# Kernel tuning notes

Measured on AMD Instinct MI355X. Metric: run time of the kernel, lower is better.

Reference implementation:

```python
import jax, jax.numpy as jnp
import numpy as np

B, T, C, H = 8, 1024, 1536, 12
D = C // H  # head_size = 128
EPS = 1e-5


def layer_norm(x, g, b):
    m = jnp.mean(x, axis=-1, keepdims=True)
    v = jnp.var(x, axis=-1, keepdims=True)
    return (x - m) / jnp.sqrt(v + EPS) * g + b


def batch_norm_T(x, g, b):
    # BatchNorm1d(block_size) on (B, T, C): channels are the T axis;
    # training-mode batch statistics over (B, C), biased variance.
    m = jnp.mean(x, axis=(0, 2), keepdims=True)
    v = jnp.var(x, axis=(0, 2), keepdims=True)
    return (x - m) / jnp.sqrt(v + EPS) * g[None, :, None] + b[None, :, None]


def setup_inputs() -> dict:
    key = jax.random.key(0)
    ks = jax.random.split(key, 12)
    s = 0.02
    inp = {
        "x": jax.random.normal(ks[0], (B, T, C), dtype=jnp.float32),
        # per-head q/k/v projections stacked: (H, C, D)
        "wq": jax.random.normal(ks[1], (H, C, D), dtype=jnp.float32) * s,
        "wk": jax.random.normal(ks[2], (H, C, D), dtype=jnp.float32) * s,
        "wv": jax.random.normal(ks[3], (H, C, D), dtype=jnp.float32) * s,
        "wo": jax.random.normal(ks[4], (C, C), dtype=jnp.float32) * s,
        "bo": jnp.zeros((C,), dtype=jnp.float32),
        "ln1_g": jnp.ones((C,), dtype=jnp.float32),
        "ln1_b": jnp.zeros((C,), dtype=jnp.float32),
        "ln2_g": jnp.ones((C,), dtype=jnp.float32),
        "ln2_b": jnp.zeros((C,), dtype=jnp.float32),
        "w1": jax.random.normal(ks[5], (C, 4 * C), dtype=jnp.float32) * s,
        "b1": jnp.zeros((4 * C,), dtype=jnp.float32),
        "w2": jax.random.normal(ks[6], (4 * C, C), dtype=jnp.float32) * s,
        "b2": jnp.zeros((C,), dtype=jnp.float32),
        "bn1_g": jnp.ones((T,), dtype=jnp.float32),
        "bn1_b": jnp.zeros((T,), dtype=jnp.float32),
        "bn2_g": jnp.ones((T,), dtype=jnp.float32),
        "bn2_b": jnp.zeros((T,), dtype=jnp.float32),
    }
    return inp


def reference(x, wq, wk, wv, wo, bo, ln1_g, ln1_b, ln2_g, ln2_b,
              w1, b1, w2, b2, bn1_g, bn1_b, bn2_g, bn2_b):
    # --- multi-head causal self-attention (pre-LN) ---
    h = layer_norm(x, ln1_g, ln1_b)                       # (B,T,C)
    q = jnp.einsum('btc,hcd->bhtd', h, wq)
    k = jnp.einsum('btc,hcd->bhtd', h, wk)
    v = jnp.einsum('btc,hcd->bhtd', h, wv)
    scores = jnp.einsum('bhtd,bhsd->bhts', q, k) * (D ** -0.5)
    causal = jnp.tril(jnp.ones((T, T), dtype=bool))
    scores = jnp.where(causal, scores, -jnp.inf)
    attn = jax.nn.softmax(scores, axis=-1)                # dropout = identity (eval)
    o = jnp.einsum('bhts,bhsd->bthd', attn, v).reshape(B, T, C)
    sa = o @ wo + bo
    x = x + sa
    x = batch_norm_T(x, bn1_g, bn1_b)
    # --- feed-forward ---
    h2 = layer_norm(x, ln2_g, ln2_b)
    ff = jax.nn.relu(h2 @ w1 + b1) @ w2 + b2
    x = batch_norm_T(x + ff, bn2_g, bn2_b)
    return x
```

## Files before the change

kernel.cpp:

```cpp
#include <hip/hip_runtime.h>
#include <hip/hip_bf16.h>

constexpr int BATCH = 8;
constexpr int SEQ   = 1024;
constexpr int CH    = 1536;
constexpr int NH    = 12;
constexpr int HD    = 128;
constexpr int FFDIM = 6144;
constexpr int NROWS = BATCH * SEQ;
constexpr int QKVLD = 3 * CH;
constexpr float EPS = 1e-5f;

typedef unsigned short ushort;
typedef __attribute__((ext_vector_type(8))) ushort us8;
typedef __attribute__((ext_vector_type(8))) __bf16 bf16x8;
typedef __attribute__((ext_vector_type(4))) float f32x4;

__device__ __forceinline__ float b2f(ushort u) {
  return __uint_as_float(((unsigned)u) << 16);
}
__device__ __forceinline__ ushort f2b(float f) {
  __hip_bfloat16 h = __float2bfloat16(f);
  return *reinterpret_cast<ushort*>(&h);
}

__device__ __forceinline__ void g2l16(const ushort* g, ushort* l) {
  __builtin_amdgcn_global_load_lds(
      (const __attribute__((address_space(1))) void*)g,
      (__attribute__((address_space(3))) void*)l, 16, 0, 0);
}

__device__ __forceinline__ float block_sum(float v, float* red) {
#pragma unroll
  for (int o = 32; o > 0; o >>= 1) v += __shfl_down(v, o, 64);
  const int w = threadIdx.x >> 6;
  if ((threadIdx.x & 63) == 0) red[w] = v;
  __syncthreads();
  const float r = red[0] + red[1] + red[2] + red[3];
  __syncthreads();
  return r;
}

__global__ __launch_bounds__(256) void ln_bf16(const float* __restrict__ x,
                                               const float* __restrict__ g,
                                               const float* __restrict__ b,
                                               ushort* __restrict__ out) {
  __shared__ float row[CH];
  __shared__ float red[4];
  const size_t base = (size_t)blockIdx.x * CH;
  float s = 0.f;
  for (int c = threadIdx.x; c < CH; c += 256) {
    const float v = x[base + c];
    row[c] = v;
    s += v;
  }
  const float mean = block_sum(s, red) * (1.0f / CH);
  float s2 = 0.f;
  for (int c = threadIdx.x; c < CH; c += 256) {
    const float d = row[c] - mean;
    s2 += d * d;
  }
  const float var = block_sum(s2, red) * (1.0f / CH);
  const float rstd = rsqrtf(var + EPS);
  for (int c = threadIdx.x; c < CH; c += 256)
    out[base + c] = f2b((row[c] - mean) * rstd * g[c] + b[c]);
}

__global__ __launch_bounds__(256) void transpose_cast(const float* __restrict__ src,
                                                      ushort* __restrict__ dst,
                                                      int R, int Cc, int ldd,
                                                      long srcZ, long dstZ) {
  __shared__ float tile[32][33];
  src += (size_t)blockIdx.z * srcZ;
  dst += (size_t)blockIdx.z * dstZ;
  const int c0 = blockIdx.x * 32, r0 = blockIdx.y * 32;
  const int tx = threadIdx.x & 31, ty = threadIdx.x >> 5;
#pragma unroll
  for (int i = ty; i < 32; i += 8)
    tile[i][tx] = src[(size_t)(r0 + i) * Cc + c0 + tx];
  __syncthreads();
#pragma unroll
  for (int i = ty; i < 32; i += 8)
    dst[(size_t)(c0 + i) * ldd + r0 + tx] = f2b(tile[tx][i]);
}

__global__ __launch_bounds__(256) void transpose_v(const ushort* __restrict__ src,
                                                   ushort* __restrict__ dst) {
  __shared__ ushort tile[32][33];
  const int bh = blockIdx.z;
  const int b = bh / NH, h = bh % NH;
  const ushort* s = src + (size_t)b * SEQ * QKVLD + (size_t)h * HD;
  ushort* d = dst + (size_t)bh * HD * SEQ;
  const int t0 = blockIdx.x * 32, d0 = blockIdx.y * 32;
  const int tx = threadIdx.x & 31, ty = threadIdx.x >> 5;
#pragma unroll
  for (int i = ty; i < 32; i += 8)
    tile[i][tx] = s[(size_t)(t0 + i) * QKVLD + d0 + tx];
  __syncthreads();
#pragma unroll
  for (int i = ty; i < 32; i += 8)
    d[(size_t)(d0 + i) * SEQ + t0 + tx] = tile[tx][i];
}

constexpr int BT = 128;
constexpr int BK = 32;

template <int RELU, int BIAS, int RES, int OUTBF>
__global__ __launch_bounds__(256) void gemm_bf16(
    const ushort* __restrict__ A, int lda,
    const ushort* __restrict__ Bt, int ldb,
    void* __restrict__ Cm, int ldc,
    const float* __restrict__ bias,
    const float* __restrict__ res, int ldr,
    int K) {
  __shared__ ushort As[BT * BK];
  __shared__ ushort Bs[BT * BK];
  const int tid = threadIdx.x;
  const int lane = tid & 63;
  const int wv = tid >> 6;
  const int m0 = blockIdx.y * BT;
  const int n0 = blockIdx.x * BT;
  const int srow = wv * 32 + (lane >> 2);
  const int schunk = (lane & 3) * 8;
  const ushort* gA0 = A + (size_t)(m0 + srow) * lda + schunk;
  const ushort* gA1 = gA0 + (size_t)16 * lda;
  const ushort* gB0 = Bt + (size_t)(n0 + srow) * ldb + schunk;
  const ushort* gB1 = gB0 + (size_t)16 * ldb;
  ushort* lA0 = As + (wv * 32) * BK;
  ushort* lA1 = lA0 + 16 * BK;
  ushort* lB0 = Bs + (wv * 32) * BK;
  ushort* lB1 = lB0 + 16 * BK;
  const int wm = (wv >> 1) * 64, wn = (wv & 1) * 64;
  const int fr = lane & 15;
  const int quad = lane >> 4;
  const int koff = quad * 8;

  f32x4 acc[4][4] = {{}};
  for (int k0 = 0; k0 < K; k0 += BK) {
    __syncthreads();
    g2l16(gA0 + k0, lA0);
    g2l16(gA1 + k0, lA1);
    g2l16(gB0 + k0, lB0);
    g2l16(gB1 + k0, lB1);
    __syncthreads();
    bf16x8 af[4], bf[4];
#pragma unroll
    for (int mi = 0; mi < 4; ++mi)
      af[mi] = *(const bf16x8*)&As[(wm + mi * 16 + fr) * BK + koff];
#pragma unroll
    for (int ni = 0; ni < 4; ++ni)
      bf[ni] = *(const bf16x8*)&Bs[(wn + ni * 16 + fr) * BK + koff];
#pragma unroll
    for (int mi = 0; mi < 4; ++mi)
#pragma unroll
      for (int ni = 0; ni < 4; ++ni)
        acc[mi][ni] = __builtin_amdgcn_mfma_f32_16x16x32_bf16(af[mi], bf[ni], acc[mi][ni], 0, 0, 0);
  }
#pragma unroll
  for (int ni = 0; ni < 4; ++ni) {
    const int col = n0 + wn + ni * 16 + fr;
    const float bs = BIAS ? bias[col] : 0.f;
#pragma unroll
    for (int mi = 0; mi < 4; ++mi) {
      const int rowb = m0 + wm + mi * 16 + quad * 4;
#pragma unroll
      for (int r = 0; r < 4; ++r) {
        float v = acc[mi][ni][r] + bs;
        if (RELU) v = fmaxf(v, 0.f);
        const size_t idx = (size_t)(rowb + r) * ldc + col;
        if (RES) v += res[(size_t)(rowb + r) * ldr + col];
        if (OUTBF) ((ushort*)Cm)[idx] = f2b(v);
        else       ((float*)Cm)[idx] = v;
      }
    }
  }
}

constexpr int FQT = 64;
constexpr int VLD = 72;

__global__ __launch_bounds__(256) void flash_attn_mfma(
    const ushort* __restrict__ q, const ushort* __restrict__ k,
    const ushort* __restrict__ vt, ushort* __restrict__ o,
    int ld, int ldo) {
  __shared__ ushort Ks[2][64 * 128];
  __shared__ ushort Vs[2][128 * 64];
  __shared__ ushort Ps[4][16][VLD];
  const int tid = threadIdx.x;
  const int lane = tid & 63;
  const int w = tid >> 6;
  const int fr = lane & 15;
  const int quad = lane >> 4;
  const int qt = blockIdx.x;
  const int b = blockIdx.y / NH;
  const int h = blockIdx.y % NH;
  const size_t base = (size_t)b * SEQ * ld + (size_t)h * HD;
  const ushort* vtb = vt + (size_t)(b * NH + h) * HD * SEQ;
  const int q0 = qt * FQT;
  const int qrow = q0 + w * 16;
  const float scale = 0.08838834764831845f;

  const ushort* gk[4];
  const ushort* gv[4];
#pragma unroll
  for (int t = 0; t < 4; ++t) {
    const int jr = w * 16 + t * 4 + (lane >> 4);
    const int kc = (lane & 15) ^ (jr & 7);
    gk[t] = k + base + (size_t)jr * ld + kc * 8;
    const int dr = w * 32 + t * 8 + (lane >> 3);
    const int vc = (lane & 7) ^ (dr & 7);
    gv[t] = vtb + (size_t)dr * SEQ + vc * 8;
  }

  bf16x8 aq[4];
  {
    const ushort* qp = q + base + (size_t)(qrow + fr) * ld + quad * 8;
#pragma unroll
    for (int ks = 0; ks < 4; ++ks) aq[ks] = *(const bf16x8*)(qp + ks * 32);
  }

  float m_i[4], l_i[4];
  f32x4 oacc[8];
#pragma unroll
  for (int i = 0; i < 4; ++i) { m_i[i] = -3.0e38f; l_i[i] = 0.f; }
#pragma unroll
  for (int n8 = 0; n8 < 8; ++n8) oacc[n8] = (f32x4){0.f, 0.f, 0.f, 0.f};

#pragma unroll
  for (int t = 0; t < 4; ++t) {
    g2l16(gk[t], &Ks[0][w * 2048 + t * 512]);
    g2l16(gv[t], &Vs[0][w * 2048 + t * 512]);
  }
  __syncthreads();

  int cur = 0;
  for (int jt = 0; jt <= qt; ++jt) {
    const int j0 = jt * FQT;
    if (jt < qt) {
      const size_t ko = (size_t)(jt + 1) * FQT * ld;
      const int vo = (jt + 1) * FQT;
      ushort* kd = (cur ? &Ks[0][0] : &Ks[1][0]) + w * 2048;
      ushort* vd = (cur ? &Vs[0][0] : &Vs[1][0]) + w * 2048;
#pragma unroll
      for (int t = 0; t < 4; ++t) {
        g2l16(gk[t] + ko, kd + t * 512);
        g2l16(gv[t] + vo, vd + t * 512);
      }
    }
    const ushort* Kc = cur ? &Ks[1][0] : &Ks[0][0];
    const ushort* Vc = cur ? &Vs[1][0] : &Vs[0][0];

    f32x4 sacc[4];
#pragma unroll
    for (int ni = 0; ni < 4; ++ni) sacc[ni] = (f32x4){0.f, 0.f, 0.f, 0.f};
#pragma unroll
    for (int ks = 0; ks < 4; ++ks) {
#pragma unroll
      for (int ni = 0; ni < 4; ++ni) {
        const int j = ni * 16 + fr;
        const int s = (ks * 4 + quad) ^ (fr & 7);
        const bf16x8 kf = *(const bf16x8*)&Kc[j * 128 + s * 8];
        sacc[ni] = __builtin_amdgcn_mfma_f32_16x16x32_bf16(aq[ks], kf, sacc[ni], 0, 0, 0);
      }
    }
    const bool diag = (jt == qt);
    float alpha[4];
#pragma unroll
    for (int i = 0; i < 4; ++i) {
      const int qg = qrow + quad * 4 + i;
      float pv[4];
      float vmax = -3.0e38f;
#pragma unroll
      for (int ni = 0; ni < 4; ++ni) {
        float sv = sacc[ni][i] * scale;
        if (diag && (j0 + ni * 16 + fr > qg)) sv = -3.0e38f;
        pv[ni] = sv;
        vmax = fmaxf(vmax, sv);
      }
#pragma unroll
      for (int mm = 8; mm >= 1; mm >>= 1) vmax = fmaxf(vmax, __shfl_xor(vmax, mm, 64));
      const float m_new = fmaxf(m_i[i], vmax);
      alpha[i] = __expf(m_i[i] - m_new);
      m_i[i] = m_new;
      float rsum = 0.f;
#pragma unroll
      for (int ni = 0; ni < 4; ++ni) {
        const float pe = __expf(pv[ni] - m_new);
        Ps[w][quad * 4 + i][ni * 16 + fr] = f2b(pe);
        rsum += pe;
      }
#pragma unroll
      for (int mm = 8; mm >= 1; mm >>= 1) rsum += __shfl_xor(rsum, mm, 64);
      l_i[i] = l_i[i] * alpha[i] + rsum;
#pragma unroll
      for (int n8 = 0; n8 < 8; ++n8) oacc[n8][i] *= alpha[i];
    }
#pragma unroll
    for (int js = 0; js < 2; ++js) {
      const bf16x8 pf = *(const bf16x8*)&Ps[w][fr][js * 32 + quad * 8];
#pragma unroll
      for (int n8 = 0; n8 < 8; ++n8) {
        const int d = n8 * 16 + fr;
        const int s = (js * 4 + quad) ^ (fr & 7);
        const bf16x8 vf = *(const bf16x8*)&Vc[d * 64 + s * 8];
        oacc[n8] = __builtin_amdgcn_mfma_f32_16x16x32_bf16(pf, vf, oacc[n8], 0, 0, 0);
      }
    }
    __syncthreads();
    cur ^= 1;
  }
#pragma unroll
  for (int i = 0; i < 4; ++i) {
    const float inv = 1.0f / l_i[i];
    ushort* op = o + ((size_t)b * SEQ + qrow + quad * 4 + i) * ldo + (size_t)h * HD;
#pragma unroll
    for (int n8 = 0; n8 < 8; ++n8) op[n8 * 16 + fr] = f2b(oacc[n8][i] * inv);
  }
}

__global__ __launch_bounds__(256) void bn_stats(const float* __restrict__ x,
                                                float* __restrict__ mean,
                                                float* __restrict__ rstd) {
  __shared__ float red[4];
  const int t = blockIdx.x;
  float s = 0.f;
  for (int bb = 0; bb < BATCH; ++bb) {
    const float* p = x + ((size_t)bb * SEQ + t) * CH;
    for (int c = threadIdx.x; c < CH; c += 256) s += p[c];
  }
  const float m = block_sum(s, red) * (1.0f / (BATCH * CH));
  float s2 = 0.f;
  for (int bb = 0; bb < BATCH; ++bb) {
    const float* p = x + ((size_t)bb * SEQ + t) * CH;
    for (int c = threadIdx.x; c < CH; c += 256) {
      const float d = p[c] - m;
      s2 += d * d;
    }
  }
  const float var = block_sum(s2, red) * (1.0f / (BATCH * CH));
  if (threadIdx.x == 0) {
    mean[t] = m;
    rstd[t] = rsqrtf(var + EPS);
  }
}

__global__ __launch_bounds__(256) void bn_apply(const float* __restrict__ x,
                                                float* __restrict__ out,
                                                const float* __restrict__ mean,
                                                const float* __restrict__ rstd,
                                                const float* __restrict__ g,
                                                const float* __restrict__ bb) {
  const size_t i = (size_t)blockIdx.x * 256 + threadIdx.x;
  const int t = (int)((i / CH) % SEQ);
  out[i] = (x[i] - mean[t]) * rstd[t] * g[t] + bb[t];
}

extern "C" void kernel_launch(void* const* d_in, const int* in_sizes, int n_in,
                              void* d_out, int out_size, void* d_ws, size_t ws_size,
                              hipStream_t stream) {
  const float* x    = (const float*)d_in[0];
  const float* wq   = (const float*)d_in[1];
  const float* wk   = (const float*)d_in[2];
  const float* wv   = (const float*)d_in[3];
  const float* wo   = (const float*)d_in[4];
  const float* bo   = (const float*)d_in[5];
  const float* ln1g = (const float*)d_in[6];
  const float* ln1b = (const float*)d_in[7];
  const float* ln2g = (const float*)d_in[8];
  const float* ln2b = (const float*)d_in[9];
  const float* w1   = (const float*)d_in[10];
  const float* b1   = (const float*)d_in[11];
  const float* w2   = (const float*)d_in[12];
  const float* b2   = (const float*)d_in[13];
  const float* bn1g = (const float*)d_in[14];
  const float* bn1b = (const float*)d_in[15];
  const float* bn2g = (const float*)d_in[16];
  const float* bn2b = (const float*)d_in[17];
  float* out = (float*)d_out;

  ushort* wsu = (ushort*)d_ws;
  const size_t NCs   = (size_t)NROWS * CH;
  ushort* R0    = wsu;
  ushort* QKV   = wsu + NCs;
  ushort* wqkvT = wsu + NCs + (size_t)NROWS * QKVLD;
  ushort* woT   = wqkvT + (size_t)QKVLD * CH;
  float*  meanp = (float*)(woT + (size_t)CH * CH);
  float*  rstdp = meanp + SEQ;
  ushort* w1T   = QKV;
  ushort* w2T   = QKV + (size_t)FFDIM * CH;
  ushort* FF1   = QKV + 2 * (size_t)FFDIM * CH;

  const dim3 blk(256);

  transpose_cast<<<dim3(HD / 32, CH / 32, NH), blk, 0, stream>>>(
      wq, wqkvT, CH, HD, CH, (long)CH * HD, (long)HD * CH);
  transpose_cast<<<dim3(HD / 32, CH / 32, NH), blk, 0, stream>>>(
      wk, wqkvT + (size_t)CH * CH, CH, HD, CH, (long)CH * HD, (long)HD * CH);
  transpose_cast<<<dim3(HD / 32, CH / 32, NH), blk, 0, stream>>>(
      wv, wqkvT + 2 * (size_t)CH * CH, CH, HD, CH, (long)CH * HD, (long)HD * CH);
  transpose_cast<<<dim3(CH / 32, CH / 32, 1), blk, 0, stream>>>(
      wo, woT, CH, CH, CH, 0, 0);

  ln_bf16<<<NROWS, blk, 0, stream>>>(x, ln1g, ln1b, R0);

  gemm_bf16<0, 0, 0, 1><<<dim3(QKVLD / BT, NROWS / BT), blk, 0, stream>>>(
      R0, CH, wqkvT, CH, QKV, QKVLD, nullptr, nullptr, 0, CH);

  transpose_v<<<dim3(SEQ / 32, HD / 32, BATCH * NH), blk, 0, stream>>>(
      QKV + 2 * CH, R0);

  flash_attn_mfma<<<dim3(SEQ / FQT, BATCH * NH), blk, 0, stream>>>(
      QKV, QKV + CH, R0, QKV, QKVLD, QKVLD);

  gemm_bf16<0, 1, 1, 0><<<dim3(CH / BT, NROWS / BT), blk, 0, stream>>>(
      QKV, QKVLD, woT, CH, out, CH, bo, x, CH, CH);

  transpose_cast<<<dim3(FFDIM / 32, CH / 32, 1), blk, 0, stream>>>(
      w1, w1T, CH, FFDIM, CH, 0, 0);
  transpose_cast<<<dim3(CH / 32, FFDIM / 32, 1), blk, 0, stream>>>(
      w2, w2T, FFDIM, CH, FFDIM, 0, 0);

  bn_stats<<<SEQ, blk, 0, stream>>>(out, meanp, rstdp);
  bn_apply<<<(NROWS * CH) / 256, blk, 0, stream>>>(out, out, meanp, rstdp, bn1g, bn1b);

  ln_bf16<<<NROWS, blk, 0, stream>>>(out, ln2g, ln2b, R0);

  constexpr int FFC = 4096;
  for (int c = 0; c < NROWS / FFC; ++c) {
    const size_t r0 = (size_t)c * FFC;
    gemm_bf16<1, 1, 0, 1><<<dim3(FFDIM / BT, FFC / BT), blk, 0, stream>>>(
        R0 + r0 * CH, CH, w1T, CH, FF1, FFDIM, b1, nullptr, 0, CH);
    gemm_bf16<0, 1, 1, 0><<<dim3(CH / BT, FFC / BT), blk, 0, stream>>>(
        FF1, FFDIM, w2T, FFDIM, out + r0 * CH, CH, b2, out + r0 * CH, CH, FFDIM);
  }

  bn_stats<<<SEQ, blk, 0, stream>>>(out, meanp, rstdp);
  bn_apply<<<(NROWS * CH) / 256, blk, 0, stream>>>(out, out, meanp, rstdp, bn2g, bn2b);
}
```

Baseline: 1.277 ms.

## Double-buffer GEMM LDS tiles, swizzle LDS layout, split-K FFN2 with atomics

The bf16 GEMM now prefetches the next K tile into a second LDS buffer while computing the current one, with one barrier per iteration instead of two. LDS chunk offsets are XOR-swizzled by row to reduce bank conflicts on fragment reads. The second FFN GEMM is split along K into two slices that atomically accumulate into the output, which already holds the residual; only the first slice adds bias. The split raises block count for the under-filled GEMM but adds atomic traffic and makes the summation order nondeterministic.

```diff
diff --git a/kernel.cpp b/kernel.cpp
--- a/kernel.cpp
+++ b/kernel.cpp
@@ -105,7 +105,7 @@
 constexpr int BT = 128;
 constexpr int BK = 32;
 
-template <int RELU, int BIAS, int RES, int OUTBF>
+template <int RELU, int BIAS, int RES, int OUTBF, int ATOMIC = 0>
 __global__ __launch_bounds__(256) void gemm_bf16(
     const ushort* __restrict__ A, int lda,
     const ushort* __restrict__ Bt, int ldb,
@@ -113,53 +113,65 @@
     const float* __restrict__ bias,
     const float* __restrict__ res, int ldr,
     int K) {
-  __shared__ ushort As[BT * BK];
-  __shared__ ushort Bs[BT * BK];
+  __shared__ ushort As[2][BT * BK];
+  __shared__ ushort Bs[2][BT * BK];
   const int tid = threadIdx.x;
   const int lane = tid & 63;
   const int wv = tid >> 6;
   const int m0 = blockIdx.y * BT;
   const int n0 = blockIdx.x * BT;
+  if (ATOMIC) {
+    const size_t kz = (size_t)blockIdx.z * K;
+    A += kz;
+    Bt += kz;
+  }
   const int srow = wv * 32 + (lane >> 2);
-  const int schunk = (lane & 3) * 8;
+  const int sx = (srow >> 1) & 3;
+  const int schunk = ((lane & 3) ^ sx) * 8;
   const ushort* gA0 = A + (size_t)(m0 + srow) * lda + schunk;
   const ushort* gA1 = gA0 + (size_t)16 * lda;
   const ushort* gB0 = Bt + (size_t)(n0 + srow) * ldb + schunk;
   const ushort* gB1 = gB0 + (size_t)16 * ldb;
-  ushort* lA0 = As + (wv * 32) * BK;
-  ushort* lA1 = lA0 + 16 * BK;
-  ushort* lB0 = Bs + (wv * 32) * BK;
-  ushort* lB1 = lB0 + 16 * BK;
+  const int lofs = (wv * 32) * BK;
   const int wm = (wv >> 1) * 64, wn = (wv & 1) * 64;
   const int fr = lane & 15;
   const int quad = lane >> 4;
-  const int koff = quad * 8;
+  const int koff = (quad ^ ((fr >> 1) & 3)) * 8;
 
   f32x4 acc[4][4] = {{}};
+  g2l16(gA0, &As[0][lofs]);
+  g2l16(gA1, &As[0][lofs + 16 * BK]);
+  g2l16(gB0, &Bs[0][lofs]);
+  g2l16(gB1, &Bs[0][lofs + 16 * BK]);
+  __syncthreads();
+  int buf = 0;
   for (int k0 = 0; k0 < K; k0 += BK) {
-    __syncthreads();
-    g2l16(gA0 + k0, lA0);
-    g2l16(gA1 + k0, lA1);
-    g2l16(gB0 + k0, lB0);
-    g2l16(gB1 + k0, lB1);
-    __syncthreads();
+    const int nk = k0 + BK;
+    if (nk < K) {
+      g2l16(gA0 + nk, &As[buf ^ 1][lofs]);
+      g2l16(gA1 + nk, &As[buf ^ 1][lofs + 16 * BK]);
+      g2l16(gB0 + nk, &Bs[buf ^ 1][lofs]);
+      g2l16(gB1 + nk, &Bs[buf ^ 1][lofs + 16 * BK]);
+    }
     bf16x8 af[4], bf[4];
 #pragma unroll
     for (int mi = 0; mi < 4; ++mi)
-      af[mi] = *(const bf16x8*)&As[(wm + mi * 16 + fr) * BK + koff];
+      af[mi] = *(const bf16x8*)&As[buf][(wm + mi * 16 + fr) * BK + koff];
 #pragma unroll
     for (int ni = 0; ni < 4; ++ni)
-      bf[ni] = *(const bf16x8*)&Bs[(wn + ni * 16 + fr) * BK + koff];
+      bf[ni] = *(const bf16x8*)&Bs[buf][(wn + ni * 16 + fr) * BK + koff];
 #pragma unroll
     for (int mi = 0; mi < 4; ++mi)
 #pragma unroll
       for (int ni = 0; ni < 4; ++ni)
         acc[mi][ni] = __builtin_amdgcn_mfma_f32_16x16x32_bf16(af[mi], bf[ni], acc[mi][ni], 0, 0, 0);
+    __syncthreads();
+    buf ^= 1;
   }
 #pragma unroll
   for (int ni = 0; ni < 4; ++ni) {
     const int col = n0 + wn + ni * 16 + fr;
-    const float bs = BIAS ? bias[col] : 0.f;
+    const float bs = (BIAS && (!ATOMIC || blockIdx.z == 0)) ? bias[col] : 0.f;
 #pragma unroll
     for (int mi = 0; mi < 4; ++mi) {
       const int rowb = m0 + wm + mi * 16 + quad * 4;
@@ -169,8 +181,9 @@
         if (RELU) v = fmaxf(v, 0.f);
         const size_t idx = (size_t)(rowb + r) * ldc + col;
         if (RES) v += res[(size_t)(rowb + r) * ldr + col];
-        if (OUTBF) ((ushort*)Cm)[idx] = f2b(v);
-        else       ((float*)Cm)[idx] = v;
+        if (ATOMIC)      atomicAdd((float*)Cm + idx, v);
+        else if (OUTBF)  ((ushort*)Cm)[idx] = f2b(v);
+        else             ((float*)Cm)[idx] = v;
       }
     }
   }
@@ -430,8 +443,8 @@
     const size_t r0 = (size_t)c * FFC;
     gemm_bf16<1, 1, 0, 1><<<dim3(FFDIM / BT, FFC / BT), blk, 0, stream>>>(
         R0 + r0 * CH, CH, w1T, CH, FF1, FFDIM, b1, nullptr, 0, CH);
-    gemm_bf16<0, 1, 1, 0><<<dim3(CH / BT, FFC / BT), blk, 0, stream>>>(
-        FF1, FFDIM, w2T, FFDIM, out + r0 * CH, CH, b2, out + r0 * CH, CH, FFDIM);
+    gemm_bf16<0, 1, 0, 0, 1><<<dim3(CH / BT, FFC / BT, 2), blk, 0, stream>>>(
+        FF1, FFDIM, w2T, FFDIM, out + r0 * CH, CH, b2, nullptr, 0, FFDIM / 2);
   }
 
   bn_stats<<<SEQ, blk, 0, stream>>>(out, meanp, rstdp);
```

Result: faster. 1.182 ms (-7.5%).
